# Performance work log

Measured on AMD Instinct MI355X. Metric: run time of the kernel, lower is better.

The kernel has to match this reference:

```python
import jax, jax.numpy as jnp
import numpy as np

B, L, D, H = 4, 2048, 1024, 16
DK = D // H


def setup_inputs() -> dict:
    key = jax.random.key(0)
    ks = jax.random.split(key, 8)
    def n(k, shape, s=1.0):
        return jax.random.normal(k, shape, dtype=jnp.float32) * s
    return {
        "q": n(ks[0], (B, L, D)),
        "k": n(ks[1], (B, L, D)),
        "v": n(ks[2], (B, L, D)),
        "Wq": n(ks[3], (D, D), 0.02), "bq": jnp.zeros((D,), jnp.float32),
        "Wk": n(ks[4], (D, D), 0.02), "bk": jnp.zeros((D,), jnp.float32),
        "Wv": n(ks[5], (D, D), 0.02), "bv": jnp.zeros((D,), jnp.float32),
        "Wo": n(ks[6], (D, D), 0.02), "bo": jnp.zeros((D,), jnp.float32),
        # relative-position table, torch: nn.Parameter(zeros(2L-1, d_k)); random here
        "w_rel": n(ks[7], (2 * L - 1, DK), 0.02),
    }


def reference(q, k, v, Wq, bq, Wk, bk, Wv, bv, Wo, bo, w_rel):
    # Dropout is identity in eval mode (reference baseline).
    bs, Lq, _ = q.shape
    qh = (q @ Wq.T + bq).reshape(bs, Lq, H, DK).transpose(0, 2, 1, 3)  # (B,H,L,dk)
    kh = (k @ Wk.T + bk).reshape(bs, -1, H, DK).transpose(0, 2, 1, 3)
    vh = (v @ Wv.T + bv).reshape(bs, -1, H, DK).transpose(0, 2, 1, 3)

    # content-content scores
    scores = jnp.einsum('bhid,bhjd->bhij', qh, kh)  # (B,H,L,L)

    # relative bias. torch unfold: rel_pos[i, d, j] = w_rel[i + j, d]
    # bias[b,h,i,j] = sum_d qh[b,h,i,d] * w_rel[i+j, d]
    # Compute t = q . w_rel over the 2L-1 axis, then skew-gather (avoids LxLxdk tensor).
    t = jnp.einsum('bhid,rd->bhir', qh, w_rel)  # (B,H,L,2L-1)
    idx = jnp.arange(Lq)[:, None] + jnp.arange(Lq)[None, :]  # (L,L) values i+j
    bias = jnp.take_along_axis(t, idx[None, None], axis=-1)  # (B,H,L,L)

    attn = jax.nn.softmax((scores + bias) / jnp.sqrt(jnp.float32(DK)), axis=-1)
    out = jnp.einsum('bhij,bhjd->bhid', attn, vh)  # (B,H,L,dk)
    concat = out.transpose(0, 2, 1, 3).reshape(bs, Lq, D)
    return concat @ Wo.T + bo
```

## Files before the change

### kernel.cpp

```cpp
#include <hip/hip_runtime.h>

typedef __attribute__((ext_vector_type(8))) short bf16x8;
typedef __attribute__((ext_vector_type(4))) float f32x4;
typedef unsigned short u16;
typedef unsigned int u32;

constexpr int kB = 4, kL = 2048, kD = 1024, kH = 16, kDK = 64;
constexpr int kR = kB * kL;
constexpr long kWrelMax = 2 * kL - 2;
constexpr float kQScale = 0.125f * 1.44269504088896f;
constexpr float kM = 12.0f;

__device__ inline float fexp2(float x) { return __builtin_amdgcn_exp2f(x); }

__device__ inline u16 f2bf(float x) {
    union { float f; u32 u; } v; v.f = x;
    u32 r = v.u + 0x7FFFu + ((v.u >> 16) & 1u);
    return (u16)(r >> 16);
}
__device__ inline float bf2f(u16 h) {
    union { u32 u; float f; } v; v.u = ((u32)h) << 16;
    return v.f;
}
__device__ inline void splitf(float x, u16& hi, u16& lo) {
    union { float f; u32 u; } v; v.f = x;
    u32 hu = v.u & 0xFFFF0000u;
    hi = (u16)(hu >> 16);
    union { u32 u; float f; } hf; hf.u = hu;
    union { float f; u32 u; } l; l.f = x - hf.f;
    lo = (u16)(l.u >> 16);
}
__device__ inline f32x4 MFMA(bf16x8 a, bf16x8 b, f32x4 c) {
    return __builtin_amdgcn_mfma_f32_16x16x32_bf16(a, b, c, 0, 0, 0);
}
__device__ __forceinline__ void gll16(const u16* g, u16* l) {
    __builtin_amdgcn_global_load_lds(
        (const __attribute__((address_space(1))) u32*)g,
        (__attribute__((address_space(3))) u32*)l, 16, 0, 0);
}

__global__ void split4x4_kernel(const float* __restrict__ i0, const float* __restrict__ i1,
                                const float* __restrict__ i2, const float* __restrict__ i3,
                                u16* __restrict__ h0, u16* __restrict__ h1,
                                u16* __restrict__ h2, u16* __restrict__ h3,
                                u16* __restrict__ l0, u16* __restrict__ l1,
                                u16* __restrict__ l2, u16* __restrict__ l3, int n4) {
    int idx = blockIdx.x * blockDim.x + threadIdx.x;
    if (idx >= n4) return;
    const float* in = blockIdx.y == 0 ? i0 : blockIdx.y == 1 ? i1 : blockIdx.y == 2 ? i2 : i3;
    u16* hi = blockIdx.y == 0 ? h0 : blockIdx.y == 1 ? h1 : blockIdx.y == 2 ? h2 : h3;
    u16* lo = blockIdx.y == 0 ? l0 : blockIdx.y == 1 ? l1 : blockIdx.y == 2 ? l2 : l3;
    float4 x = reinterpret_cast<const float4*>(in)[idx];
    ushort4 h, l;
    splitf(x.x, h.x, l.x); splitf(x.y, h.y, l.y);
    splitf(x.z, h.z, l.z); splitf(x.w, h.w, l.w);
    reinterpret_cast<ushort4*>(hi)[idx] = h;
    reinterpret_cast<ushort4*>(lo)[idx] = l;
}
__global__ void split4_kernel(const float* __restrict__ in,
                              u16* __restrict__ hi, u16* __restrict__ lo, int n4) {
    int idx = blockIdx.x * blockDim.x + threadIdx.x;
    if (idx >= n4) return;
    float4 x = reinterpret_cast<const float4*>(in)[idx];
    ushort4 h, l;
    splitf(x.x, h.x, l.x); splitf(x.y, h.y, l.y);
    splitf(x.z, h.z, l.z); splitf(x.w, h.w, l.w);
    reinterpret_cast<ushort4*>(hi)[idx] = h;
    reinterpret_cast<ushort4*>(lo)[idx] = l;
}

template<int AMODE, int OMODE, int TERMS>
__global__ __launch_bounds__(256) void mfma_gemm(
    const float* __restrict__ Af32,
    const u16* __restrict__ Agh, const u16* __restrict__ Agl,
    const u16* __restrict__ Bgh, const u16* __restrict__ Bgl,
    const float* __restrict__ bias, float scale,
    float* __restrict__ Yf, u16* __restrict__ Yh, u16* __restrict__ Yl)
{
    __shared__ __align__(16) u16 Ash[128 * 32], Asl[128 * 32];
    __shared__ __align__(16) u16 Bsh[128 * 32];
    __shared__ __align__(16) u16 Bsl[TERMS == 3 ? 128 * 32 : 8];

    const int tid = threadIdx.x;
    const int row0 = blockIdx.x * 128, col0 = blockIdx.y * 128;
    const int w = tid >> 6, lane = tid & 63;
    const int s = lane & 15, g = lane >> 4;
    const int wrow = w >> 1, wcol = w & 1;
    const int srow = tid >> 1;
    const int skq  = (tid & 1) * 16;

    const f32x4 fz = {0.f, 0.f, 0.f, 0.f};
    f32x4 acc[4][4];
    #pragma unroll
    for (int m = 0; m < 4; ++m)
        #pragma unroll
        for (int n = 0; n < 4; ++n) acc[m][n] = fz;

    float4 aR[4];
    bf16x8 aRh[2], aRl[2], bRh[2], bRl[2];

    auto loadA = [&](int k0) {
        if (AMODE == 0) {
            const float* p = &Af32[(size_t)(row0 + srow) * kD + k0 + skq];
            aR[0] = *(const float4*)(p);
            aR[1] = *(const float4*)(p + 4);
            aR[2] = *(const float4*)(p + 8);
            aR[3] = *(const float4*)(p + 12);
        } else {
            const u16* ph = &Agh[(size_t)(row0 + srow) * kD + k0 + skq];
            const u16* pl = &Agl[(size_t)(row0 + srow) * kD + k0 + skq];
            aRh[0] = *(const bf16x8*)ph; aRh[1] = *(const bf16x8*)(ph + 8);
            aRl[0] = *(const bf16x8*)pl; aRl[1] = *(const bf16x8*)(pl + 8);
        }
    };
    auto loadB = [&](int k0) {
        const u16* ph = &Bgh[(size_t)(col0 + srow) * kD + k0 + skq];
        bRh[0] = *(const bf16x8*)ph; bRh[1] = *(const bf16x8*)(ph + 8);
        if (TERMS == 3) {
            const u16* pl = &Bgl[(size_t)(col0 + srow) * kD + k0 + skq];
            bRl[0] = *(const bf16x8*)pl; bRl[1] = *(const bf16x8*)(pl + 8);
        }
    };
    auto writeAB = [&]() {
        const int c0 = skq >> 3, sw = srow & 3;
        bf16x8 h0, h1, l0, l1;
        if (AMODE == 0) {
            const float* af = (const float*)aR;
            #pragma unroll
            for (int q = 0; q < 8; ++q) {
                u16 hh, ll;
                splitf(af[q], hh, ll);     h0[q] = (short)hh; l0[q] = (short)ll;
                splitf(af[8 + q], hh, ll); h1[q] = (short)hh; l1[q] = (short)ll;
            }
        } else { h0 = aRh[0]; h1 = aRh[1]; l0 = aRl[0]; l1 = aRl[1]; }
        *(bf16x8*)&Ash[srow * 32 + (((c0    ) ^ sw) << 3)] = h0;
        *(bf16x8*)&Ash[srow * 32 + (((c0 + 1) ^ sw) << 3)] = h1;
        *(bf16x8*)&Asl[srow * 32 + (((c0    ) ^ sw) << 3)] = l0;
        *(bf16x8*)&Asl[srow * 32 + (((c0 + 1) ^ sw) << 3)] = l1;
        *(bf16x8*)&Bsh[srow * 32 + (((c0    ) ^ sw) << 3)] = bRh[0];
        *(bf16x8*)&Bsh[srow * 32 + (((c0 + 1) ^ sw) << 3)] = bRh[1];
        if (TERMS == 3) {
            *(bf16x8*)&Bsl[srow * 32 + (((c0    ) ^ sw) << 3)] = bRl[0];
            *(bf16x8*)&Bsl[srow * 32 + (((c0 + 1) ^ sw) << 3)] = bRl[1];
        }
    };

    loadA(0); loadB(0);
    for (int k0 = 0; k0 < kD; k0 += 32) {
        __syncthreads();
        writeAB();
        __syncthreads();
        if (k0 + 32 < kD) { loadA(k0 + 32); loadB(k0 + 32); }

        bf16x8 fAh[4], fAl[4], fBh[4], fBl[4];
        #pragma unroll
        for (int m = 0; m < 4; ++m) {
            int ar = wrow * 64 + m * 16 + s;
            int off = ar * 32 + ((g ^ (ar & 3)) << 3);
            fAh[m] = *(const bf16x8*)&Ash[off];
            fAl[m] = *(const bf16x8*)&Asl[off];
        }
        #pragma unroll
        for (int n = 0; n < 4; ++n) {
            int bc = wcol * 64 + n * 16 + s;
            int off = bc * 32 + ((g ^ (bc & 3)) << 3);
            fBh[n] = *(const bf16x8*)&Bsh[off];
            if (TERMS == 3) fBl[n] = *(const bf16x8*)&Bsl[off];
        }
        #pragma unroll
        for (int m = 0; m < 4; ++m)
            #pragma unroll
            for (int n = 0; n < 4; ++n) {
                acc[m][n] = MFMA(fAh[m], fBh[n], acc[m][n]);
                acc[m][n] = MFMA(fAl[m], fBh[n], acc[m][n]);
                if (TERMS == 3) acc[m][n] = MFMA(fAh[m], fBl[n], acc[m][n]);
            }
    }

    #pragma unroll
    for (int n = 0; n < 4; ++n) {
        const int colg = col0 + wcol * 64 + n * 16 + s;
        const float bv = bias[colg];
        #pragma unroll
        for (int m = 0; m < 4; ++m) {
            const int rowg = row0 + wrow * 64 + m * 16 + (g << 2);
            if (OMODE == 3) {
                const int b = rowg >> 11, i = rowg & (kL - 1);
                const int h = colg >> 6, d = colg & 63;
                ushort4 o4;
                o4.x = f2bf(acc[m][n][0] + bv);
                o4.y = f2bf(acc[m][n][1] + bv);
                o4.z = f2bf(acc[m][n][2] + bv);
                o4.w = f2bf(acc[m][n][3] + bv);
                *(ushort4*)&Yh[(((size_t)b * kH + h) * kDK + d) * kL + i] = o4;
            } else {
                #pragma unroll
                for (int r = 0; r < 4; ++r) {
                    float val = (acc[m][n][r] + bv) * scale;
                    if (OMODE == 1) {
                        Yf[(size_t)(rowg + r) * kD + colg] = val;
                    } else {
                        const int rg = rowg + r;
                        const int b = rg >> 11, i = rg & (kL - 1);
                        const int h = colg >> 6, d = colg & 63;
                        size_t o = (((size_t)b * kH + h) * kL + i) * kDK + d;
                        Yh[o] = f2bf(val);
                    }
                }
            }
        }
    }
}

__global__ __launch_bounds__(256, 2) void attn3(
    const u16* __restrict__ Qh,
    const u16* __restrict__ Kg, const u16* __restrict__ VT,
    const u16* __restrict__ Wr,
    u16* __restrict__ Ch, u16* __restrict__ Cl)
{
    __shared__ __align__(16) u16 Ksh[2][64 * 64];
    __shared__ __align__(16) u16 Vsh[2][64 * 64];
    __shared__ __align__(16) u16 Wsh[2][64 * 64];
    __shared__ __align__(16) u16 Ps[4][16 * 64];
    __shared__ __align__(16) u16 Tb[4][128 * 20];

    const int tid = threadIdx.x;
    const int w = tid >> 6, lane = tid & 63;
    const int s = lane & 15, g = lane >> 4;
    const int bh = blockIdx.y, i0 = blockIdx.x * 64;
    const int b = bh >> 4, h = bh & 15;

    const int srow = tid >> 3;
    const int sc = tid & 7;

    auto stageK = [&](int buf, int t) {
        const u16* base = Kg + ((size_t)bh * kL + (size_t)t * 64) * kDK;
        #pragma unroll
        for (int it = 0; it < 2; ++it) {
            int r = srow + it * 32;
            gll16(base + r * 64 + ((sc ^ (r & 7)) << 3), &Ksh[buf][it * 2048 + w * 512]);
        }
    };
    auto stageV = [&](int buf, int t) {
        #pragma unroll
        for (int it = 0; it < 2; ++it) {
            int d = srow + it * 32;
            const u16* src = VT + ((size_t)bh * kDK + d) * kL + t * 64 + ((sc ^ (d & 7)) << 3);
            gll16(src, &Vsh[buf][it * 2048 + w * 512]);
        }
    };
    auto stageW = [&](int buf, int c) {
        #pragma unroll
        for (int it = 0; it < 2; ++it) {
            int r = srow + it * 32;
            long row = (long)i0 + 64L * c + r;
            if (row > kWrelMax) row = kWrelMax;
            gll16(Wr + row * 64 + ((sc ^ (r & 7)) << 3), &Wsh[buf][it * 2048 + w * 512]);
        }
    };

    int foff[4][2];
    #pragma unroll
    for (int n = 0; n < 4; ++n)
        #pragma unroll
        for (int ks = 0; ks < 2; ++ks) {
            int row = n * 16 + s;
            foff[n][ks] = row * 64 + (((ks * 4 + g) ^ (row & 7)) << 3);
        }
    int prd[2];
    #pragma unroll
    for (int ks = 0; ks < 2; ++ks)
        prd[ks] = s * 64 + (((ks * 4 + g) ^ (s & 7)) << 3);
    int pwoff[4][4];
    #pragma unroll
    for (int jn = 0; jn < 4; ++jn)
        #pragma unroll
        for (int r = 0; r < 4; ++r) {
            int il = g * 4 + r, j = jn * 16 + s;
            pwoff[jn][r] = il * 64 + (((j >> 3) ^ (il & 7)) << 3) + (j & 7);
        }

    const size_t qbase = ((size_t)bh * kL + i0 + w * 16 + s) * kDK + g * 8;
    bf16x8 qh[2];
    qh[0] = *(const bf16x8*)&Qh[qbase];
    qh[1] = *(const bf16x8*)&Qh[qbase + 32];

    auto computeT = [&](int c, int buf) {
        const f32x4 fz = {0.f, 0.f, 0.f, 0.f};
        f32x4 tacc[4] = {fz, fz, fz, fz};
        #pragma unroll
        for (int un = 0; un < 4; ++un)
            #pragma unroll
            for (int ks = 0; ks < 2; ++ks) {
                bf16x8 wf = *(const bf16x8*)&Wsh[buf][foff[un][ks]];
                tacc[un] = MFMA(qh[ks], wf, tacc[un]);
            }
        const int cb = c * 64 + s - g * 4;
        #pragma unroll
        for (int un = 0; un < 4; ++un)
            #pragma unroll
            for (int r = 0; r < 4; ++r) {
                int key = (cb + un * 16 - r) & 127;
                Tb[w][key * 20 + g * 4 + r] =
                    (u16)(__float_as_uint(tacc[un][r]) >> 16);
            }
    };

    stageK(0, 0); stageV(0, 0); stageW(0, 0); stageW(1, 1);
    __syncthreads();
    computeT(0, 0); computeT(1, 1);
    __syncthreads();

    float lS[4] = {0.f, 0.f, 0.f, 0.f};
    const f32x4 fz = {0.f, 0.f, 0.f, 0.f};
    f32x4 oacc[4] = {fz, fz, fz, fz};

    for (int t = 0; t < 32; ++t) {
        const int cur = t & 1, nxt = cur ^ 1;
        if (t < 31) {
            stageK(nxt, t + 1);
            stageV(nxt, t + 1);
            stageW(cur, t + 2);
        }
        if (t >= 1) computeT(t + 1, nxt);

        f32x4 sacc[4] = {fz, fz, fz, fz};
        __builtin_amdgcn_s_setprio(1);
        #pragma unroll
        for (int jn = 0; jn < 4; ++jn)
            #pragma unroll
            for (int ks = 0; ks < 2; ++ks) {
                bf16x8 kf = *(const bf16x8*)&Ksh[cur][foff[jn][ks]];
                sacc[jn] = MFMA(qh[ks], kf, sacc[jn]);
            }
        __builtin_amdgcn_s_setprio(0);

        #pragma unroll
        for (int jn = 0; jn < 4; ++jn) {
            int key = (w * 16 + t * 64 + jn * 16 + s) & 127;
            ushort4 tv = *(const ushort4*)&Tb[w][key * 20 + g * 4];
            sacc[jn][0] += bf2f(tv.x);
            sacc[jn][1] += bf2f(tv.y);
            sacc[jn][2] += bf2f(tv.z);
            sacc[jn][3] += bf2f(tv.w);
        }

        #pragma unroll
        for (int jn = 0; jn < 4; ++jn)
            #pragma unroll
            for (int r = 0; r < 4; ++r) {
                float p = fexp2(sacc[jn][r] - kM);
                u32 pu = __float_as_uint(p) & 0xFFFF0000u;
                lS[r] += __uint_as_float(pu);
                Ps[w][pwoff[jn][r]] = (u16)(pu >> 16);
            }

        __builtin_amdgcn_s_setprio(1);
        #pragma unroll
        for (int ks = 0; ks < 2; ++ks) {
            bf16x8 pf = *(const bf16x8*)&Ps[w][prd[ks]];
            #pragma unroll
            for (int dn = 0; dn < 4; ++dn) {
                bf16x8 vf = *(const bf16x8*)&Vsh[cur][foff[dn][ks]];
                oacc[dn] = MFMA(pf, vf, oacc[dn]);
            }
        }
        __builtin_amdgcn_s_setprio(0);
        __syncthreads();
    }

    float inv[4];
    #pragma unroll
    for (int r = 0; r < 4; ++r) {
        float ps = lS[r];
        ps += __shfl_xor(ps, 1);
        ps += __shfl_xor(ps, 2);
        ps += __shfl_xor(ps, 4);
        ps += __shfl_xor(ps, 8);
        inv[r] = 1.0f / ps;
    }
    #pragma unroll
    for (int dn = 0; dn < 4; ++dn)
        #pragma unroll
        for (int r = 0; r < 4; ++r) {
            const int ig = i0 + w * 16 + g * 4 + r;
            float val = oacc[dn][r] * inv[r];
            u16 hh, ll; splitf(val, hh, ll);
            size_t o = ((size_t)(b * kL + ig)) * kD + h * kDK + dn * 16 + s;
            Ch[o] = hh; Cl[o] = ll;
        }
}

extern "C" void kernel_launch(void* const* d_in, const int* in_sizes, int n_in,
                              void* d_out, int out_size, void* d_ws, size_t ws_size,
                              hipStream_t stream) {
    const float* q    = (const float*)d_in[0];
    const float* k    = (const float*)d_in[1];
    const float* v    = (const float*)d_in[2];
    const float* Wq   = (const float*)d_in[3];
    const float* bq   = (const float*)d_in[4];
    const float* Wk   = (const float*)d_in[5];
    const float* bk   = (const float*)d_in[6];
    const float* Wv   = (const float*)d_in[7];
    const float* bv   = (const float*)d_in[8];
    const float* Wo   = (const float*)d_in[9];
    const float* bo   = (const float*)d_in[10];
    const float* wrel = (const float*)d_in[11];
    float* out = (float*)d_out;

    u16* p = (u16*)d_ws;
    const size_t nW = (size_t)kD * kD;
    const size_t nR = (size_t)(2 * kL - 1) * kDK;
    const size_t nT = (size_t)kB * kL * kD;
    u16* wqh = p; p += nW;  u16* wql = p; p += nW;
    u16* wkh = p; p += nW;  u16* wkl = p; p += nW;
    u16* wvh = p; p += nW;  u16* wvl = p; p += nW;
    u16* woh = p; p += nW;  u16* wol = p; p += nW;
    u16* wrh = p; p += nR;  u16* wrl = p; p += nR;
    u16* qhh = p; p += nT;
    u16* khh = p; p += nT;
    u16* vT  = p; p += nT;
    u16* cch = p; p += nT;  u16* ccl = p; p += nT;

    hipLaunchKernelGGL(split4x4_kernel, dim3(1024, 4), dim3(256), 0, stream,
                       Wq, Wk, Wv, Wo, wqh, wkh, wvh, woh, wql, wkl, wvl, wol,
                       (int)(nW / 4));
    hipLaunchKernelGGL(split4_kernel, dim3(256), dim3(256), 0, stream,
                       wrel, wrh, wrl, (int)(nR / 4));

    dim3 blk(256);
    dim3 gP(kR / 128, kD / 128);
    hipLaunchKernelGGL((mfma_gemm<0, 2, 2>), gP, blk, 0, stream,
                       q, nullptr, nullptr, wqh, wql, bq, kQScale, nullptr, qhh, nullptr);
    hipLaunchKernelGGL((mfma_gemm<0, 2, 2>), gP, blk, 0, stream,
                       k, nullptr, nullptr, wkh, wkl, bk, 1.0f, nullptr, khh, nullptr);
    hipLaunchKernelGGL((mfma_gemm<0, 3, 2>), gP, blk, 0, stream,
                       v, nullptr, nullptr, wvh, wvl, bv, 1.0f, nullptr, vT, nullptr);

    hipLaunchKernelGGL(attn3, dim3(kL / 64, kB * kH), blk, 0, stream,
                       qhh, khh, vT, wrh, cch, ccl);

    hipLaunchKernelGGL((mfma_gemm<1, 1, 3>), gP, blk, 0, stream,
                       nullptr, cch, ccl, woh, wol, bo, 1.0f, out, nullptr, nullptr);
}
```

Baseline: 409.8 us.

## Drop double buffering in attention kernel and raise occupancy to four blocks

Turns the K/V shared-memory double buffers into single buffers and drops the staged W_rel tile. W_rel fragments are now loaded straight from global memory into registers for the relative-bias MFMA. The per-warp bias buffer becomes one shared swizzled table, and its values seed the score accumulator instead of being added after the QK MFMA. The smaller shared-memory footprint allows launch bounds of 4 blocks per CU, relying on more resident blocks rather than in-block prefetch to hide load latency. The cost is an extra barrier per tile and no overlap of the next tile's loads within a block.

```diff
diff --git a/kernel.cpp b/kernel.cpp
--- a/kernel.cpp
+++ b/kernel.cpp
@@ -17,10 +17,6 @@
     union { float f; u32 u; } v; v.f = x;
     u32 r = v.u + 0x7FFFu + ((v.u >> 16) & 1u);
     return (u16)(r >> 16);
-}
-__device__ inline float bf2f(u16 h) {
-    union { u32 u; float f; } v; v.u = ((u32)h) << 16;
-    return v.f;
 }
 __device__ inline void splitf(float x, u16& hi, u16& lo) {
     union { float f; u32 u; } v; v.f = x;
@@ -212,17 +208,16 @@
     }
 }
 
-__global__ __launch_bounds__(256, 2) void attn3(
+__global__ __launch_bounds__(256, 4) void attn3(
     const u16* __restrict__ Qh,
     const u16* __restrict__ Kg, const u16* __restrict__ VT,
     const u16* __restrict__ Wr,
     u16* __restrict__ Ch, u16* __restrict__ Cl)
 {
-    __shared__ __align__(16) u16 Ksh[2][64 * 64];
-    __shared__ __align__(16) u16 Vsh[2][64 * 64];
-    __shared__ __align__(16) u16 Wsh[2][64 * 64];
+    __shared__ __align__(16) u16 Ksh[64 * 64];
+    __shared__ __align__(16) u16 Vsh[64 * 64];
     __shared__ __align__(16) u16 Ps[4][16 * 64];
-    __shared__ __align__(16) u16 Tb[4][128 * 20];
+    __shared__ __align__(16) u16 Tb[128 * 64];
 
     const int tid = threadIdx.x;
     const int w = tid >> 6, lane = tid & 63;
@@ -233,29 +228,20 @@
     const int srow = tid >> 3;
     const int sc = tid & 7;
 
-    auto stageK = [&](int buf, int t) {
+    auto stageK = [&](int t) {
         const u16* base = Kg + ((size_t)bh * kL + (size_t)t * 64) * kDK;
         #pragma unroll
         for (int it = 0; it < 2; ++it) {
             int r = srow + it * 32;
-            gll16(base + r * 64 + ((sc ^ (r & 7)) << 3), &Ksh[buf][it * 2048 + w * 512]);
-        }
-    };
-    auto stageV = [&](int buf, int t) {
+            gll16(base + r * 64 + ((sc ^ (r & 7)) << 3), &Ksh[it * 2048 + w * 512]);
+        }
+    };
+    auto stageV = [&](int t) {
         #pragma unroll
         for (int it = 0; it < 2; ++it) {
             int d = srow + it * 32;
             const u16* src = VT + ((size_t)bh * kDK + d) * kL + t * 64 + ((sc ^ (d & 7)) << 3);
-            gll16(src, &Vsh[buf][it * 2048 + w * 512]);
-        }
-    };
-    auto stageW = [&](int buf, int c) {
-        #pragma unroll
-        for (int it = 0; it < 2; ++it) {
-            int r = srow + it * 32;
-            long row = (long)i0 + 64L * c + r;
-            if (row > kWrelMax) row = kWrelMax;
-            gll16(Wr + row * 64 + ((sc ^ (r & 7)) << 3), &Wsh[buf][it * 2048 + w * 512]);
+            gll16(src, &Vsh[it * 2048 + w * 512]);
         }
     };
 
@@ -285,65 +271,67 @@
     qh[0] = *(const bf16x8*)&Qh[qbase];
     qh[1] = *(const bf16x8*)&Qh[qbase + 32];
 
-    auto computeT = [&](int c, int buf) {
-        const f32x4 fz = {0.f, 0.f, 0.f, 0.f};
-        f32x4 tacc[4] = {fz, fz, fz, fz};
-        #pragma unroll
-        for (int un = 0; un < 4; ++un)
-            #pragma unroll
-            for (int ks = 0; ks < 2; ++ks) {
-                bf16x8 wf = *(const bf16x8*)&Wsh[buf][foff[un][ks]];
-                tacc[un] = MFMA(qh[ks], wf, tacc[un]);
-            }
+    const f32x4 fz = {0.f, 0.f, 0.f, 0.f};
+    const int ilw = w * 16 + g * 4;
+
+    auto computeT = [&](int c) {
+        bf16x8 wf[4][2];
+        #pragma unroll
+        for (int un = 0; un < 4; ++un) {
+            long row = (long)i0 + 64L * c + un * 16 + s;
+            if (row > kWrelMax) row = kWrelMax;
+            const u16* pw = Wr + row * 64 + g * 8;
+            wf[un][0] = *(const bf16x8*)pw;
+            wf[un][1] = *(const bf16x8*)(pw + 32);
+        }
+        f32x4 tacc[4];
+        #pragma unroll
+        for (int un = 0; un < 4; ++un) {
+            tacc[un] = MFMA(qh[0], wf[un][0], fz);
+            tacc[un] = MFMA(qh[1], wf[un][1], tacc[un]);
+        }
         const int cb = c * 64 + s - g * 4;
         #pragma unroll
         for (int un = 0; un < 4; ++un)
             #pragma unroll
             for (int r = 0; r < 4; ++r) {
                 int key = (cb + un * 16 - r) & 127;
-                Tb[w][key * 20 + g * 4 + r] =
+                Tb[key * 64 + ((ilw + r) ^ ((key & 7) << 3))] =
                     (u16)(__float_as_uint(tacc[un][r]) >> 16);
             }
     };
 
-    stageK(0, 0); stageV(0, 0); stageW(0, 0); stageW(1, 1);
-    __syncthreads();
-    computeT(0, 0); computeT(1, 1);
-    __syncthreads();
+    computeT(0); computeT(1);
 
     float lS[4] = {0.f, 0.f, 0.f, 0.f};
-    const f32x4 fz = {0.f, 0.f, 0.f, 0.f};
     f32x4 oacc[4] = {fz, fz, fz, fz};
 
     for (int t = 0; t < 32; ++t) {
-        const int cur = t & 1, nxt = cur ^ 1;
-        if (t < 31) {
-            stageK(nxt, t + 1);
-            stageV(nxt, t + 1);
-            stageW(cur, t + 2);
-        }
-        if (t >= 1) computeT(t + 1, nxt);
-
-        f32x4 sacc[4] = {fz, fz, fz, fz};
-        __builtin_amdgcn_s_setprio(1);
-        #pragma unroll
-        for (int jn = 0; jn < 4; ++jn)
-            #pragma unroll
-            for (int ks = 0; ks < 2; ++ks) {
-                bf16x8 kf = *(const bf16x8*)&Ksh[cur][foff[jn][ks]];
-                sacc[jn] = MFMA(qh[ks], kf, sacc[jn]);
-            }
-        __builtin_amdgcn_s_setprio(0);
-
+        stageK(t); stageV(t);
+        if (t >= 1) computeT(t + 1);
+        __syncthreads();
+
+        f32x4 sacc[4];
         #pragma unroll
         for (int jn = 0; jn < 4; ++jn) {
             int key = (w * 16 + t * 64 + jn * 16 + s) & 127;
-            ushort4 tv = *(const ushort4*)&Tb[w][key * 20 + g * 4];
-            sacc[jn][0] += bf2f(tv.x);
-            sacc[jn][1] += bf2f(tv.y);
-            sacc[jn][2] += bf2f(tv.z);
-            sacc[jn][3] += bf2f(tv.w);
-        }
+            const u32* tp = (const u32*)&Tb[key * 64 + (ilw ^ ((key & 7) << 3))];
+            u32 w0 = tp[0], w1 = tp[1];
+            sacc[jn][0] = __uint_as_float(w0 << 16);
+            sacc[jn][1] = __uint_as_float(w0 & 0xFFFF0000u);
+            sacc[jn][2] = __uint_as_float(w1 << 16);
+            sacc[jn][3] = __uint_as_float(w1 & 0xFFFF0000u);
+        }
+
+        __builtin_amdgcn_s_setprio(1);
+        #pragma unroll
+        for (int jn = 0; jn < 4; ++jn)
+            #pragma unroll
+            for (int ks = 0; ks < 2; ++ks) {
+                bf16x8 kf = *(const bf16x8*)&Ksh[foff[jn][ks]];
+                sacc[jn] = MFMA(qh[ks], kf, sacc[jn]);
+            }
+        __builtin_amdgcn_s_setprio(0);
 
         #pragma unroll
         for (int jn = 0; jn < 4; ++jn)
@@ -361,7 +349,7 @@
             bf16x8 pf = *(const bf16x8*)&Ps[w][prd[ks]];
             #pragma unroll
             for (int dn = 0; dn < 4; ++dn) {
-                bf16x8 vf = *(const bf16x8*)&Vsh[cur][foff[dn][ks]];
+                bf16x8 vf = *(const bf16x8*)&Vsh[foff[dn][ks]];
                 oacc[dn] = MFMA(pf, vf, oacc[dn]);
             }
         }
```

Result: slower. 470.2 us (+14.7%).
